# Kernel tuning notes

Hardware: AMD Instinct MI355X
Metric: run time of the kernel (lower is better)

The kernel has to match this reference:

```python
import jax, jax.numpy as jnp
import numpy as np

B, T, N = 8, 1024, 1024
R, NR = 8, 128          # regions, neurons per region (N = R*NR)
D = 512                 # d_model


def setup_inputs() -> dict:
    key = jax.random.key(0)
    ks = jax.random.split(key, 6)
    spikes = jax.random.normal(ks[0], (B, T, N), dtype=jnp.float32)
    # region assignment: random permutation of neuron ids split into R groups
    perm = jax.random.permutation(ks[1], N)
    region_indices = perm.reshape(R, NR).astype(jnp.int32)
    # per-region Linear(NR -> D) stored already transposed for gathered layout
    W_enc = jax.random.normal(ks[2], (R, NR, D), dtype=jnp.float32) / np.sqrt(NR)
    b_enc = jax.random.normal(ks[3], (R, D), dtype=jnp.float32) * 0.02
    # per-region Linear(D -> NR)
    W_dec = jax.random.normal(ks[4], (R, D, NR), dtype=jnp.float32) / np.sqrt(D)
    b_dec = jax.random.normal(ks[5], (R, NR), dtype=jnp.float32) * 0.02
    return {"spikes": spikes, "W_enc": W_enc, "b_enc": b_enc,
            "W_dec": W_dec, "b_dec": b_dec, "region_indices": region_indices}


def reference(spikes, W_enc, b_enc, W_dec, b_dec, region_indices):
    # gather: per-region channel subsets  [B,T,R,NR]
    x_r = spikes[:, :, region_indices]
    # RegionEncoder: Linear(NR -> D) per region  [B,T,R,D]
    tokens = jnp.einsum('btrn,rnd->btrd', x_r, W_enc) + b_enc
    # RegionDecoder: Linear(D -> NR) per region  [B,T,R,NR]
    y = jnp.einsum('btrd,rdn->btrn', tokens, W_dec) + b_dec
    # scatter back into full neuron axis (index_copy_ on dim 2)
    flat_idx = region_indices.reshape(-1)          # [N], a permutation
    out = jnp.zeros_like(spikes).at[:, :, flat_idx].set(y.reshape(spikes.shape[0], spikes.shape[1], -1))
    return out
```

## Files before the change

### kernel.cpp

```cpp
#include <hip/hip_runtime.h>
#include <hip/hip_bf16.h>


typedef __attribute__((ext_vector_type(8))) short bf16x8;
typedef __attribute__((ext_vector_type(4))) float f32x4;
typedef __attribute__((ext_vector_type(4))) short s16x4;

#define NREG 8
#define NRD  128
#define DD   512
#define NN   1024
#define ROWS 16

static __device__ __forceinline__ unsigned short f2bf(float x) {
  union { float f; unsigned u; } v; v.f = x;
  unsigned r = v.u + 0x7fffu + ((v.u >> 16) & 1u);
  return (unsigned short)(r >> 16);
}
static __device__ __forceinline__ unsigned short f2bf_hw(float x) {
  union { __hip_bfloat16 h; unsigned short u; } c;
  c.h = __float2bfloat16(x);
  return c.u;
}
static __device__ __forceinline__ float bf2f(unsigned short b) {
  union { unsigned u; float f; } v; v.u = ((unsigned)b) << 16;
  return v.f;
}

__global__ __launch_bounds__(256) void prep1_kernel(
    const float* __restrict__ W_enc, const float* __restrict__ b_enc,
    const float* __restrict__ W_dec, const int* __restrict__ idx,
    int* __restrict__ pos_ws, float* __restrict__ part,
    float* __restrict__ part_c)
{
  __shared__ unsigned short As[128 * 128];
  __shared__ unsigned short Bs[128 * 128];
  int blk = blockIdx.x, t = threadIdx.x;

  if (blk < 32) {
    int r = blk >> 2, dc = blk & 3, d0 = dc * 128;
    const float* We = W_enc + (size_t)r * NRD * DD;
    const float* Wd = W_dec + (size_t)r * DD * NRD;
    const float* be = b_enc + (size_t)r * DD;

    int n4 = (t & 31) * 4, dlb = t >> 5;
    float c0 = 0.f, c1 = 0.f, c2 = 0.f, c3 = 0.f;
    #pragma unroll
    for (int p = 0; p < 16; ++p) {
      int dl = dlb + p * 8;
      float4 v = *(const float4*)&Wd[(size_t)(d0 + dl) * NRD + n4];
      float bev = be[d0 + dl];
      As[(n4 + 0) * 128 + (dl ^ (((n4 + 0) & 7) << 3))] = f2bf(v.x);
      As[(n4 + 1) * 128 + (dl ^ (((n4 + 1) & 7) << 3))] = f2bf(v.y);
      As[(n4 + 2) * 128 + (dl ^ (((n4 + 2) & 7) << 3))] = f2bf(v.z);
      As[(n4 + 3) * 128 + (dl ^ (((n4 + 3) & 7) << 3))] = f2bf(v.w);
      c0 += v.x * bev; c1 += v.y * bev; c2 += v.z * bev; c3 += v.w * bev;
    }
    {
      float4 cv; cv.x = c0; cv.y = c1; cv.z = c2; cv.w = c3;
      *(float4*)&part_c[((size_t)(r * 4 + dc) * 8 + dlb) * 128 + n4] = cv;
    }
    #pragma unroll
    for (int i = 0; i < 8; ++i) {
      int cid = t + i * 256;
      int k = cid >> 4, dq = (cid & 15) * 8;
      const float* src = &We[(size_t)k * DD + d0 + dq];
      float4 u = *(const float4*)src;
      float4 u2 = *(const float4*)(src + 4);
      bf16x8 pk;
      pk[0] = (short)f2bf(u.x);  pk[1] = (short)f2bf(u.y);
      pk[2] = (short)f2bf(u.z);  pk[3] = (short)f2bf(u.w);
      pk[4] = (short)f2bf(u2.x); pk[5] = (short)f2bf(u2.y);
      pk[6] = (short)f2bf(u2.z); pk[7] = (short)f2bf(u2.w);
      *(bf16x8*)&Bs[k * 128 + (dq ^ ((k & 7) << 3))] = pk;
    }
    __syncthreads();

    int lane = t & 63, w = t >> 6;
    int arow = lane & 15, ag = lane >> 4;
    f32x4 acc[8][2];
    #pragma unroll
    for (int i = 0; i < 8; ++i) {
      acc[i][0] = (f32x4){0.f, 0.f, 0.f, 0.f};
      acc[i][1] = (f32x4){0.f, 0.f, 0.f, 0.f};
    }
    #pragma unroll
    for (int nt = 0; nt < 8; ++nt) {
      int nl = nt * 16 + arow, asw = (nl & 7) << 3;
      bf16x8 a[4];
      #pragma unroll
      for (int ks = 0; ks < 4; ++ks)
        a[ks] = *(const bf16x8*)&As[nl * 128 + ((ks * 32 + ag * 8) ^ asw)];
      #pragma unroll
      for (int kt = 0; kt < 2; ++kt) {
        int kk = w * 32 + kt * 16 + arow, bsw = (kk & 7) << 3;
        #pragma unroll
        for (int ks = 0; ks < 4; ++ks) {
          bf16x8 b = *(const bf16x8*)&Bs[kk * 128 + ((ks * 32 + ag * 8) ^ bsw)];
          acc[nt][kt] = __builtin_amdgcn_mfma_f32_16x16x32_bf16(a[ks], b, acc[nt][kt], 0, 0, 0);
        }
      }
    }
    float* dst = part + (size_t)(r * 4 + dc) * 16384;
    #pragma unroll
    for (int nt = 0; nt < 8; ++nt)
      #pragma unroll
      for (int kt = 0; kt < 2; ++kt)
        #pragma unroll
        for (int v = 0; v < 4; ++v)
          dst[(nt * 16 + ag * 4 + v) * 128 + (w * 32 + kt * 16 + arow)] = acc[nt][kt][v];
  } else {
    #pragma unroll
    for (int i = 0; i < 4; ++i) {
      int q = t * 4 + i;
      pos_ws[idx[q]] = q;
    }
  }
}

__global__ __launch_bounds__(256) void prep2_kernel(
    const float* __restrict__ part, const float* __restrict__ part_c,
    const float* __restrict__ b_dec, unsigned short* __restrict__ MTp,
    float* __restrict__ c_ws)
{
  int blk = blockIdx.x, t = threadIdx.x;
  if (blk < 128) {
    int e0 = (blk * 256 + t) * 4;
    int r = e0 >> 14, off = e0 & 16383;
    int n = off >> 7, k0 = off & 127;
    const float* p = part + (size_t)r * 4 * 16384 + off;
    float4 s0 = *(const float4*)&p[0];
    float4 s1 = *(const float4*)&p[16384];
    float4 s2 = *(const float4*)&p[32768];
    float4 s3 = *(const float4*)&p[49152];
    s16x4 o;
    o.x = (short)f2bf(s0.x + s1.x + s2.x + s3.x);
    o.y = (short)f2bf(s0.y + s1.y + s2.y + s3.y);
    o.z = (short)f2bf(s0.z + s1.z + s2.z + s3.z);
    o.w = (short)f2bf(s0.w + s1.w + s2.w + s3.w);
    int w = n >> 4, arow = n & 15, kt = k0 >> 5, ag = (k0 >> 3) & 3, sub = k0 & 7;
    int chunk = (r * 32 + w * 4 + kt) * 64 + (arow * 4 + ag);
    *(s16x4*)&MTp[chunk * 8 + sub] = o;
  } else if (blk < 132) {
    int e = (blk - 128) * 256 + t;
    int n = e & 127;
    int r = e >> 7;
    float s = b_dec[e];
    #pragma unroll
    for (int dc = 0; dc < 4; ++dc)
      #pragma unroll
      for (int g = 0; g < 8; ++g)
        s += part_c[((size_t)(r * 4 + dc) * 8 + g) * 128 + n];
    c_ws[e] = s;
  }
}

__global__ __launch_bounds__(1024) void codec_kernel(
    const float* __restrict__ spikes, const int* __restrict__ pos_ws,
    const float* __restrict__ c_ws, const unsigned short* __restrict__ MTp,
    const int* __restrict__ idx, float* __restrict__ out)
{
  __shared__ unsigned short Xs[ROWS * NN];
  __shared__ unsigned short Ys[ROWS * NN];
  int t = threadIdx.x;
  int w = t >> 6, lane = t & 63;
  int wg = w >> 3, wcol = w & 7;
  int arow = lane & 15, ag = lane >> 4;
  int n0 = wcol * 16 + arow;
  int lanechunk = arow * 4 + ag;
  size_t row0 = (size_t)blockIdx.x * ROWS;

  int4 p4c[4];
  #pragma unroll
  for (int ch = 0; ch < 4; ++ch)
    p4c[ch] = *(const int4*)&pos_ws[ch * 256 + lane * 4];
  float cv[4];
  int col[4];
  #pragma unroll
  for (int q = 0; q < 4; ++q) {
    int r = wg * 4 + q;
    cv[q]  = c_ws[r * 128 + n0];
    col[q] = idx[r * 128 + n0];
  }

  {
    int base = w * NN, sw = (w & 7) << 3;
    #pragma unroll
    for (int ch = 0; ch < 4; ++ch) {
      int j = ch * 256 + lane * 4;
      float4 v = *(const float4*)&spikes[(row0 + w) * NN + j];
      int4 p4 = p4c[ch];
      Xs[base + (p4.x ^ sw)] = f2bf_hw(v.x);
      Xs[base + (p4.y ^ sw)] = f2bf_hw(v.y);
      Xs[base + (p4.z ^ sw)] = f2bf_hw(v.z);
      Xs[base + (p4.w ^ sw)] = f2bf_hw(v.w);
    }
  }
  __syncthreads();

  const bf16x8* Bb = (const bf16x8*)MTp;
  int asw = (arow & 7) << 3;
  #pragma unroll
  for (int q = 0; q < 4; ++q) {
    int r = wg * 4 + q;
    bf16x8 b[4], a[4];
    #pragma unroll
    for (int kt = 0; kt < 4; ++kt)
      b[kt] = Bb[(r * 32 + wcol * 4 + kt) * 64 + lanechunk];
    #pragma unroll
    for (int kt = 0; kt < 4; ++kt)
      a[kt] = *(const bf16x8*)&Xs[arow * NN + ((r * 128 + kt * 32 + ag * 8) ^ asw)];
    f32x4 acc = {0.f, 0.f, 0.f, 0.f};
    #pragma unroll
    for (int kt = 0; kt < 4; ++kt)
      acc = __builtin_amdgcn_mfma_f32_16x16x32_bf16(a[kt], b[kt], acc, 0, 0, 0);
    #pragma unroll
    for (int v = 0; v < 4; ++v) {
      int i = ag * 4 + v, isw = (i & 7) << 3;
      Ys[i * NN + (col[q] ^ isw)] = f2bf_hw(acc[v] + cv[q]);
    }
  }
  __syncthreads();

  {
    int sw = (w & 7) << 3;
    #pragma unroll
    for (int ch = 0; ch < 4; ++ch) {
      int j = ch * 256 + lane * 4;
      s16x4 y = *(const s16x4*)&Ys[w * NN + (j ^ sw)];
      float4 v;
      v.x = bf2f((unsigned short)y.x);
      v.y = bf2f((unsigned short)y.y);
      v.z = bf2f((unsigned short)y.z);
      v.w = bf2f((unsigned short)y.w);
      *(float4*)&out[(row0 + w) * NN + j] = v;
    }
  }
}

extern "C" void kernel_launch(void* const* d_in, const int* in_sizes, int n_in,
                              void* d_out, int out_size, void* d_ws, size_t ws_size,
                              hipStream_t stream) {
  const float* spikes = (const float*)d_in[0];
  const float* W_enc  = (const float*)d_in[1];
  const float* b_enc  = (const float*)d_in[2];
  const float* W_dec  = (const float*)d_in[3];
  const float* b_dec  = (const float*)d_in[4];
  const int*   idx    = (const int*)d_in[5];
  float* out = (float*)d_out;

  char* ws = (char*)d_ws;
  int*            pos_ws  = (int*)ws;
  float*          c_ws    = (float*)(ws + 4096);
  unsigned short* MTp_ws  = (unsigned short*)(ws + 8192);
  float*          part    = (float*)(ws + 270336);
  float*          part_c  = (float*)(ws + 2367488);

  prep1_kernel<<<33, 256, 0, stream>>>(W_enc, b_enc, W_dec, idx,
                                       pos_ws, part, part_c);
  prep2_kernel<<<132, 256, 0, stream>>>(part, part_c, b_dec, MTp_ws, c_ws);
  codec_kernel<<<8192 / ROWS, 1024, 0, stream>>>(spikes, pos_ws, c_ws, MTp_ws, idx, out);
}
```

Before: 32.56 us.

## Process two row tiles per block, reuse one LDS buffer, prefetch next tile

The codec kernel now handles two 16-row tiles per block (256 blocks instead of 512). It drops the separate Ys buffer by writing outputs back into Xs in permuted order, then reading them with the same pos mapping used for the gather. It also prefetches the next tile's spikes into registers while the current tile runs its MFMAs. Halving LDS use could allow more blocks per CU, but the extra barriers and fewer blocks on a 256-CU part may cut parallelism.

Measured after the change: 33.83 us. 1.04x slower.

```diff
diff --git a/kernel.cpp b/kernel.cpp
--- a/kernel.cpp
+++ b/kernel.cpp
@@ -11,6 +11,7 @@
 #define DD   512
 #define NN   1024
 #define ROWS 16
+#define TPB  2
 
 static __device__ __forceinline__ unsigned short f2bf(float x) {
   union { float f; unsigned u; } v; v.f = x;
@@ -158,82 +159,109 @@
 __global__ __launch_bounds__(1024) void codec_kernel(
     const float* __restrict__ spikes, const int* __restrict__ pos_ws,
     const float* __restrict__ c_ws, const unsigned short* __restrict__ MTp,
-    const int* __restrict__ idx, float* __restrict__ out)
+    float* __restrict__ out)
 {
   __shared__ unsigned short Xs[ROWS * NN];
-  __shared__ unsigned short Ys[ROWS * NN];
   int t = threadIdx.x;
   int w = t >> 6, lane = t & 63;
   int wg = w >> 3, wcol = w & 7;
   int arow = lane & 15, ag = lane >> 4;
   int n0 = wcol * 16 + arow;
   int lanechunk = arow * 4 + ag;
-  size_t row0 = (size_t)blockIdx.x * ROWS;
+  int asw = (arow & 7) << 3;
+  int rsw = (w & 7) << 3;
+  size_t row0 = (size_t)blockIdx.x * (ROWS * TPB);
 
   int4 p4c[4];
   #pragma unroll
   for (int ch = 0; ch < 4; ++ch)
     p4c[ch] = *(const int4*)&pos_ws[ch * 256 + lane * 4];
   float cv[4];
-  int col[4];
-  #pragma unroll
-  for (int q = 0; q < 4; ++q) {
-    int r = wg * 4 + q;
-    cv[q]  = c_ws[r * 128 + n0];
-    col[q] = idx[r * 128 + n0];
-  }
-
-  {
-    int base = w * NN, sw = (w & 7) << 3;
+  #pragma unroll
+  for (int q = 0; q < 4; ++q)
+    cv[q] = c_ws[(wg * 4 + q) * 128 + n0];
+
+  const bf16x8* Bb = (const bf16x8*)MTp;
+
+  #pragma unroll
+  for (int ch = 0; ch < 4; ++ch) {
+    int j = ch * 256 + lane * 4;
+    float4 v = *(const float4*)&spikes[(row0 + w) * NN + j];
+    int4 p4 = p4c[ch];
+    int base = w * NN;
+    Xs[base + (p4.x ^ rsw)] = f2bf_hw(v.x);
+    Xs[base + (p4.y ^ rsw)] = f2bf_hw(v.y);
+    Xs[base + (p4.z ^ rsw)] = f2bf_hw(v.z);
+    Xs[base + (p4.w ^ rsw)] = f2bf_hw(v.w);
+  }
+  __syncthreads();
+
+  float4 pv[4];
+  #pragma unroll
+  for (int tt = 0; tt < TPB; ++tt) {
+    size_t rowc = row0 + (size_t)tt * ROWS;
+
+    if (tt + 1 < TPB) {
+      #pragma unroll
+      for (int ch = 0; ch < 4; ++ch)
+        pv[ch] = *(const float4*)&spikes[(rowc + ROWS + w) * NN + ch * 256 + lane * 4];
+    }
+
+    f32x4 acc[4];
+    #pragma unroll
+    for (int q = 0; q < 4; ++q) {
+      int r = wg * 4 + q;
+      bf16x8 b[4], a[4];
+      #pragma unroll
+      for (int kt = 0; kt < 4; ++kt)
+        b[kt] = Bb[(r * 32 + wcol * 4 + kt) * 64 + lanechunk];
+      #pragma unroll
+      for (int kt = 0; kt < 4; ++kt)
+        a[kt] = *(const bf16x8*)&Xs[arow * NN + ((r * 128 + kt * 32 + ag * 8) ^ asw)];
+      acc[q] = (f32x4){0.f, 0.f, 0.f, 0.f};
+      #pragma unroll
+      for (int kt = 0; kt < 4; ++kt)
+        acc[q] = __builtin_amdgcn_mfma_f32_16x16x32_bf16(a[kt], b[kt], acc[q], 0, 0, 0);
+    }
+    __syncthreads();
+
+    #pragma unroll
+    for (int q = 0; q < 4; ++q) {
+      int r = wg * 4 + q;
+      #pragma unroll
+      for (int v = 0; v < 4; ++v) {
+        int i = ag * 4 + v, isw = (i & 7) << 3;
+        Xs[i * NN + ((r * 128 + n0) ^ isw)] = f2bf_hw(acc[q][v] + cv[q]);
+      }
+    }
+    __syncthreads();
+
     #pragma unroll
     for (int ch = 0; ch < 4; ++ch) {
       int j = ch * 256 + lane * 4;
-      float4 v = *(const float4*)&spikes[(row0 + w) * NN + j];
       int4 p4 = p4c[ch];
-      Xs[base + (p4.x ^ sw)] = f2bf_hw(v.x);
-      Xs[base + (p4.y ^ sw)] = f2bf_hw(v.y);
-      Xs[base + (p4.z ^ sw)] = f2bf_hw(v.z);
-      Xs[base + (p4.w ^ sw)] = f2bf_hw(v.w);
-    }
-  }
-  __syncthreads();
-
-  const bf16x8* Bb = (const bf16x8*)MTp;
-  int asw = (arow & 7) << 3;
-  #pragma unroll
-  for (int q = 0; q < 4; ++q) {
-    int r = wg * 4 + q;
-    bf16x8 b[4], a[4];
-    #pragma unroll
-    for (int kt = 0; kt < 4; ++kt)
-      b[kt] = Bb[(r * 32 + wcol * 4 + kt) * 64 + lanechunk];
-    #pragma unroll
-    for (int kt = 0; kt < 4; ++kt)
-      a[kt] = *(const bf16x8*)&Xs[arow * NN + ((r * 128 + kt * 32 + ag * 8) ^ asw)];
-    f32x4 acc = {0.f, 0.f, 0.f, 0.f};
-    #pragma unroll
-    for (int kt = 0; kt < 4; ++kt)
-      acc = __builtin_amdgcn_mfma_f32_16x16x32_bf16(a[kt], b[kt], acc, 0, 0, 0);
-    #pragma unroll
-    for (int v = 0; v < 4; ++v) {
-      int i = ag * 4 + v, isw = (i & 7) << 3;
-      Ys[i * NN + (col[q] ^ isw)] = f2bf_hw(acc[v] + cv[q]);
-    }
-  }
-  __syncthreads();
-
-  {
-    int sw = (w & 7) << 3;
-    #pragma unroll
-    for (int ch = 0; ch < 4; ++ch) {
-      int j = ch * 256 + lane * 4;
-      s16x4 y = *(const s16x4*)&Ys[w * NN + (j ^ sw)];
+      int base = w * NN;
       float4 v;
-      v.x = bf2f((unsigned short)y.x);
-      v.y = bf2f((unsigned short)y.y);
-      v.z = bf2f((unsigned short)y.z);
-      v.w = bf2f((unsigned short)y.w);
-      *(float4*)&out[(row0 + w) * NN + j] = v;
+      v.x = bf2f(Xs[base + (p4.x ^ rsw)]);
+      v.y = bf2f(Xs[base + (p4.y ^ rsw)]);
+      v.z = bf2f(Xs[base + (p4.z ^ rsw)]);
+      v.w = bf2f(Xs[base + (p4.w ^ rsw)]);
+      *(float4*)&out[(rowc + w) * NN + j] = v;
+    }
+
+    if (tt + 1 < TPB) {
+      __syncthreads();
+      #pragma unroll
+      for (int ch = 0; ch < 4; ++ch) {
+        int4 p4 = p4c[ch];
+        int base = w * NN;
+        float4 v = pv[ch];
+        Xs[base + (p4.x ^ rsw)] = f2bf_hw(v.x);
+        Xs[base + (p4.y ^ rsw)] = f2bf_hw(v.y);
+        Xs[base + (p4.z ^ rsw)] = f2bf_hw(v.z);
+        Xs[base + (p4.w ^ rsw)] = f2bf_hw(v.w);
+      }
+      __syncthreads();
     }
   }
 }
@@ -259,5 +287,5 @@
   prep1_kernel<<<33, 256, 0, stream>>>(W_enc, b_enc, W_dec, idx,
                                        pos_ws, part, part_c);
   prep2_kernel<<<132, 256, 0, stream>>>(part, part_c, b_dec, MTp_ws, c_ws);
-  codec_kernel<<<8192 / ROWS, 1024, 0, stream>>>(spikes, pos_ws, c_ws, MTp_ws, idx, out);
-}
+  codec_kernel<<<8192 / (ROWS * TPB), 1024, 0, stream>>>(spikes, pos_ws, c_ws, MTp_ws, out);
+}
```
